# Kernel optimization log

Measured on AMD Instinct MI355X. Metric: run time of the kernel, lower is better.

The kernel has to match this reference:

```python
import jax, jax.numpy as jnp
import numpy as np

B, S, T = 1024, 1024, 32
TAGS = ["O"] + [p + f"T{i}" for i in range(1, 16) for p in ("B-", "I-")] + ["B-T16"]
MASKED = -1.0e4


def _init_params(key):
    bound = float(np.sqrt(6.0 / T))
    k1, k2, k3 = jax.random.split(key, 3)
    start = np.array(jax.random.uniform(k1, (T,), minval=-bound, maxval=bound))
    trans = np.array(jax.random.uniform(k2, (T, T), minval=-bound, maxval=bound))
    end = np.array(jax.random.uniform(k3, (T,), minval=-bound, maxval=bound))
    # structural BIO masking, as in _initialize_parameters
    for i, src in enumerate(TAGS):
        if src.startswith("I-"):
            start[i] = MASKED
        for j, tgt in enumerate(TAGS):
            if (src.startswith("B-") or src.startswith("I-")) and tgt.startswith("I-") and src[2:] != tgt[2:]:
                trans[i, j] = MASKED
            elif src == "O" and tgt.startswith("I-"):
                trans[i, j] = MASKED
    return jnp.asarray(start, jnp.float32), jnp.asarray(trans, jnp.float32), jnp.asarray(end, jnp.float32)


def setup_inputs() -> dict:
    key = jax.random.key(0)
    k_em, k_tag, k_len, k_par = jax.random.split(key, 4)
    emissions = jax.random.normal(k_em, (B, S, T), dtype=jnp.float32)
    tags = jax.random.randint(k_tag, (B, S), 0, T, dtype=jnp.int64) if jax.config.jax_enable_x64 else jax.random.randint(k_tag, (B, S), 0, T).astype(jnp.int32)
    lengths = jax.random.randint(k_len, (B,), S // 4, S + 1)
    mask = jnp.arange(S)[None, :] < lengths[:, None]  # prefix mask, bool [B, S]
    start_transitions, transitions, end_transitions = _init_params(k_par)
    return {
        "emissions": emissions,
        "tags": tags,
        "mask": mask,
        "start_transitions": start_transitions,
        "transitions": transitions,
        "end_transitions": end_transitions,
    }


def reference(emissions, tags, mask, start_transitions, transitions, end_transitions):
    b, s, t = emissions.shape
    ar = jnp.arange(s)
    bidx = jnp.arange(b)
    head = jnp.min(jnp.where(mask, ar[None, :], s - 1), axis=1)  # [B]
    tail = jnp.max(ar[None, :] * mask, axis=1)                   # [B]
    nonempty = mask.sum(axis=1) != 0

    # condition[:, j-1] == (mask[:, j] and head != j), for j = 1..S-1
    cond = mask[:, 1:] & (head[:, None] != ar[None, 1:])  # [B, S-1]

    # ---- numerator (gold path score): additive, fully vectorized ----
    head_tags = tags[bidx, head]
    tail_tags = tags[bidx, tail]
    em_tag = jnp.take_along_axis(emissions, tags[:, :, None], axis=2)[:, :, 0]  # [B, S]
    trans_step = transitions[tags[:, :-1], tags[:, 1:]]                          # [B, S-1]
    numerator = (start_transitions[head_tags]
                 + em_tag[bidx, head]
                 + jnp.sum(jnp.where(cond, trans_step + em_tag[:, 1:], 0.0), axis=1)
                 + end_transitions[tail_tags])
    numerator = jnp.where(nonempty, numerator, 0.0)

    # ---- denominator (log partition): scan over time ----
    score0 = start_transitions[None, :] + emissions[bidx, head]  # [B, T]

    def step(score, xs):
        em_j, cond_j = xs  # [B, T], [B]
        nxt = jax.nn.logsumexp(score[:, :, None] + transitions[None, :, :] + em_j[:, None, :], axis=1)
        return jnp.where(cond_j[:, None], nxt, score), None

    em_seq = jnp.moveaxis(emissions[:, 1:, :], 1, 0)  # [S-1, B, T]
    cond_seq = jnp.moveaxis(cond, 1, 0)               # [S-1, B]
    score_final, _ = jax.lax.scan(step, score0, (em_seq, cond_seq))
    denominator = jax.nn.logsumexp(score_final + end_transitions[None, :], axis=1)
    denominator = jnp.where(nonempty, denominator, 0.0)

    # ---- token_mean reduction ----
    llh = denominator - numerator
    labels = mask.sum(axis=1).astype(emissions.dtype)
    eps = 1e-6
    return jnp.sum(llh / (labels + eps)) / (jnp.sum(labels != 0).astype(emissions.dtype) + eps)
```

## Files before the change

### kernel.cpp

```cpp
#include <hip/hip_runtime.h>
#include <cstdint>

static constexpr int S = 1024;
static constexpr int T = 32;
static constexpr float L2E  = 1.4426950408889634f;
static constexpr float LN2f = 0.6931471805599453f;

typedef __attribute__((ext_vector_type(8)))  short  short8;
typedef __attribute__((ext_vector_type(16))) float  float16;

union Frag { unsigned u[4]; short8 s; };

__global__ void crf_zero(float* ws) {
  ws[0] = 0.0f; ws[1] = 0.0f; ((unsigned*)ws)[2] = 0u;
}

__device__ __forceinline__ float bcast_lane(float v, int k) {
  return __uint_as_float((unsigned)__builtin_amdgcn_readlane((int)__float_as_uint(v), k));
}

__device__ __forceinline__ unsigned cvtpk(float lo, float hi) {
  unsigned r;
  asm("v_cvt_pk_bf16_f32 %0, %1, %2" : "=v"(r) : "v"(lo), "v"(hi));
  return r;
}

__device__ __forceinline__ int sig(int k) {
  int g2 = (k >> 2) & 3;
  if (g2 == 1) g2 = 2; else if (g2 == 2) g2 = 1;
  return (k & ~12) | (g2 << 2);
}

__global__ __launch_bounds__(512, 8) void crf_main(
    const float* __restrict__ em, const int* __restrict__ tags,
    const int* __restrict__ mask, const float* __restrict__ startT,
    const float* __restrict__ trans, const float* __restrict__ endT,
    float* __restrict__ ws, float* __restrict__ out, int B)
{
  __shared__ __align__(16) float    s_g32[8 * 512];
  __shared__ __align__(16) unsigned s_mats[8 * 544];
  __shared__ float s_trans[1024];
  __shared__ short s_tags[1024];
  __shared__ unsigned long long s_mb[17];
  __shared__ int   s_head, s_tail, s_cnt, s_K[8];
  __shared__ float s_num[8];

  const int tid = threadIdx.x;
  const int l   = tid & 63;
  const int wv  = tid >> 6;
  const int b   = blockIdx.x;
  const int n   = l & 31;
  const int h   = l >> 5;

  const float* emb   = em   + (size_t)b * S * T;
  const int*   maskb = mask + (size_t)b * S;
  const int*   tagsb = tags + (size_t)b * S;

  for (int i = tid; i < 1024; i += 512) {
    s_tags[i]  = (short)tagsb[i];
    s_trans[i] = trans[i];
  }
  {
    unsigned long long b0 = __ballot(maskb[wv * 128 + l] != 0);
    unsigned long long b1 = __ballot(maskb[wv * 128 + 64 + l] != 0);
    if (l == 0) { s_mb[2 * wv] = b0; s_mb[2 * wv + 1] = b1; }
    if (tid == 0) s_mb[16] = 0ull;
  }

  Frag Alo, Ahi;
  #pragma unroll
  for (int p = 0; p < 4; ++p) {
    int k0 = 8 * h + 2 * p;
    Alo.u[p] = cvtpk(exp2f(trans[sig(k0 + 0)      * T + n] * L2E),
                     exp2f(trans[sig(k0 + 1)      * T + n] * L2E));
    Ahi.u[p] = cvtpk(exp2f(trans[sig(16 + k0 + 0) * T + n] * L2E),
                     exp2f(trans[sig(16 + k0 + 1) * T + n] * L2E));
  }
  __syncthreads();

  if (wv == 0) {
    int first = 0x7fffffff, last = -1, pc = 0;
    if (l < 16) {
      unsigned long long w = s_mb[l];
      if (w) {
        first = 64 * l + (int)__builtin_ctzll(w);
        last  = 64 * l + 63 - (int)__builtin_clzll(w);
        pc    = (int)__builtin_popcountll(w);
      }
    }
    #pragma unroll
    for (int d = 1; d < 64; d <<= 1) {
      first = min(first, __shfl_xor(first, d));
      last  = max(last,  __shfl_xor(last,  d));
      pc   += __shfl_xor(pc, d);
    }
    if (l == 0) { s_head = first; s_tail = last; s_cnt = pc; }
  }
  __syncthreads();
  const int cnt  = s_cnt;
  const int head = (cnt > 0) ? s_head : 0;
  const int tail = (cnt > 0) ? s_tail : 0;

  const int span = tail - head;
  const int Lc   = (span + 7) >> 3;
  const int c0   = head + 1 + wv * Lc;
  const int c1   = min(c0 + Lc, tail + 1);

  float* sgw32 = s_g32 + wv * 512;
  Frag Blo, Bhi;
  #pragma unroll
  for (int p = 0; p < 4; ++p) {
    int k0 = 8 * h + 2 * p;
    Blo.u[p] = ((sig(k0) == n)          ? 0x3F80u : 0u) |
               ((sig(k0 + 1) == n)      ? 0x3F800000u : 0u);
    Bhi.u[p] = ((sig(16 + k0) == n)     ? 0x3F80u : 0u) |
               ((sig(16 + k0 + 1) == n) ? 0x3F800000u : 0u);
  }
  int   Kacc  = 0;
  float numer = 0.0f;

  float4 v0, v1;
#define LOADEM(J0) do {                                                      \
    const int r0_ = min((J0) + (l >> 3),     S - 1);                         \
    const int r1_ = min((J0) + 8 + (l >> 3), S - 1);                         \
    v0 = ((const float4*)(emb + (size_t)r0_ * T))[l & 7];                    \
    v1 = ((const float4*)(emb + (size_t)r1_ * T))[l & 7];                    \
  } while (0)

#define STOREG() do {                                                        \
    float4 g0_, g1_;                                                         \
    g0_.x = exp2f(v0.x * L2E); g0_.y = exp2f(v0.y * L2E);                    \
    g0_.z = exp2f(v0.z * L2E); g0_.w = exp2f(v0.w * L2E);                    \
    g1_.x = exp2f(v1.x * L2E); g1_.y = exp2f(v1.y * L2E);                    \
    g1_.z = exp2f(v1.z * L2E); g1_.w = exp2f(v1.w * L2E);                    \
    ((float4*)sgw32)[l] = g0_; ((float4*)sgw32)[l + 64] = g1_;               \
  } while (0)

#define FOLD(JJ, RSC) do {                                                   \
    const float4* gw = (const float4*)(sgw32 + (JJ) * 32);                   \
    float4 wa = gw[h], wb = gw[h + 2], wc = gw[h + 4], wd = gw[h + 6];       \
    float16 D = {0,0,0,0,0,0,0,0,0,0,0,0,0,0,0,0};                           \
    D = __builtin_amdgcn_mfma_f32_32x32x16_bf16(Alo.s, Blo.s, D, 0, 0, 0);   \
    D = __builtin_amdgcn_mfma_f32_32x32x16_bf16(Ahi.s, Bhi.s, D, 0, 0, 0);   \
    D[0]  *= wa.x; D[1]  *= wa.y; D[2]  *= wa.z; D[3]  *= wa.w;              \
    D[4]  *= wb.x; D[5]  *= wb.y; D[6]  *= wb.z; D[7]  *= wb.w;              \
    D[8]  *= wc.x; D[9]  *= wc.y; D[10] *= wc.z; D[11] *= wc.w;              \
    D[12] *= wd.x; D[13] *= wd.y; D[14] *= wd.z; D[15] *= wd.w;              \
    if (RSC) {                                                               \
      float mx = fmaxf(fmaxf(fmaxf(D[0], D[1]), fmaxf(D[2], D[3])),          \
                       fmaxf(fmaxf(D[4], D[5]), fmaxf(D[6], D[7])));         \
      mx = fmaxf(mx, fmaxf(fmaxf(fmaxf(D[8], D[9]),  fmaxf(D[10], D[11])),   \
                           fmaxf(fmaxf(D[12], D[13]), fmaxf(D[14], D[15]))));\
      mx = fmaxf(mx, __shfl_xor(mx, 32));             \
      mx = __uint_as_float((unsigned)__builtin_amdgcn_readfirstlane(         \
               (int)__float_as_uint(mx)));                                   \
      int E = (int)((__float_as_uint(mx) >> 23) & 0xffu);                    \
      float sc = __uint_as_float((unsigned)(254 - E) << 23);                 \
      Kacc += E - 127;                                                       \
      _Pragma("unroll")                                                      \
      for (int q_ = 0; q_ < 16; ++q_) D[q_] *= sc;                           \
    }                                                                        \
    Blo.u[0] = cvtpk(D[0],  D[1]);  Blo.u[1] = cvtpk(D[2],  D[3]);           \
    Blo.u[2] = cvtpk(D[4],  D[5]);  Blo.u[3] = cvtpk(D[6],  D[7]);           \
    Bhi.u[0] = cvtpk(D[8],  D[9]);  Bhi.u[1] = cvtpk(D[10], D[11]);          \
    Bhi.u[2] = cvtpk(D[12], D[13]); Bhi.u[3] = cvtpk(D[14], D[15]);          \
  } while (0)

  if (c0 < c1) LOADEM(c0);

  for (int j0 = c0; j0 < c1; j0 += 16) {
    const int ns = min(16, c1 - j0);

    STOREG();
    if (j0 + 16 < c1) LOADEM(j0 + 16);

    const int w = j0 >> 6, o = j0 & 63;
    unsigned long long bits = s_mb[w] >> o;
    if (o) bits |= s_mb[w + 1] << (64 - o);
    unsigned eff = (unsigned)(bits & 0xFFFFull) & (unsigned)((1u << ns) - 1u);

    if (l < ns && ((eff >> l) & 1u)) {
      int j  = j0 + l;
      int tg = (int)s_tags[j], tp = (int)s_tags[j - 1];
      float gval = sgw32[l * 32 + tg];
      numer += s_trans[tp * T + tg] + log2f(gval) * LN2f;
    }

    if (eff == 0xFFFFu) {
      #pragma unroll
      for (int jj = 0; jj < 16; ++jj) FOLD(jj, ((jj & 7) == 7));
    } else {
      for (int jj = 0; jj < ns; ++jj)
        if ((eff >> jj) & 1u) FOLD(jj, true);
    }
  }
#undef FOLD
#undef STOREG
#undef LOADEM

  {
    unsigned* mw = s_mats + wv * 544;
    #pragma unroll
    for (int p = 0; p < 4; ++p) {
      mw[(sig(8 * h + 2 * p)      >> 1) * 34 + n] = Blo.u[p];
      mw[(sig(16 + 8 * h + 2 * p) >> 1) * 34 + n] = Bhi.u[p];
    }
  }
  #pragma unroll
  for (int d = 1; d < 64; d <<= 1) numer += __shfl_xor(numer, d);
  if (l == 0) { s_num[wv] = numer; s_K[wv] = Kacc; }
  __syncthreads();

  if (wv == 0) {
    const int t = n;
    const float em0 = emb[head * T + t];
    float sc0 = (startT[t] + em0) * L2E;
    float m0 = sc0;
    #pragma unroll
    for (int d = 1; d < 32; d <<= 1) m0 = fmaxf(m0, __shfl_xor(m0, d));
    float e = exp2f(sc0 - m0);
    float Mtot = m0;

    const unsigned sh = (t & 1) ? 0u : 16u;
    for (int c = 0; c < 8; ++c) {
      const unsigned* mw = s_mats + c * 544 + (t >> 1) * 34;
      float acc = 0.0f;
      #pragma unroll
      for (int q2 = 0; q2 < 16; ++q2) {
        uint2 w2 = *(const uint2*)(mw + 2 * q2);
        float vlo = __uint_as_float((w2.x << sh) & 0xFFFF0000u);
        float vhi = __uint_as_float((w2.y << sh) & 0xFFFF0000u);
        acc = fmaf(vlo, bcast_lane(e, 2 * q2), acc);
        acc = fmaf(vhi, bcast_lane(e, 2 * q2 + 1), acc);
      }
      e = acc;
      Mtot += (float)s_K[c];
      float mx = e;
      #pragma unroll
      for (int d = 1; d < 32; d <<= 1) mx = fmaxf(mx, __shfl_xor(mx, d));
      int E = (int)((__float_as_uint(mx) >> 23) & 0xffu);
      e *= __uint_as_float((unsigned)(254 - E) << 23);
      Mtot += (float)(E - 127);
    }

    float fv = e * exp2f(endT[t] * L2E);
    #pragma unroll
    for (int d = 1; d < 32; d <<= 1) fv += __shfl_xor(fv, d);
    float denom = (Mtot + log2f(fv)) * LN2f;

    if (l == 0) {
      if (cnt > 0) {
        float ntot = 0.0f;
        for (int wq = 0; wq < 8; ++wq) ntot += s_num[wq];
        int th = (int)s_tags[head], tt = (int)s_tags[tail];
        ntot += startT[th] + bcast_lane(em0, th) + endT[tt];
        atomicAdd(&ws[0], (denom - ntot) / ((float)cnt + 1e-6f));
        atomicAdd(&ws[1], 1.0f);
      }
      __threadfence();
      unsigned done = atomicAdd((unsigned*)ws + 2, 1u);
      if (done == (unsigned)(B - 1)) {
        __threadfence();
        out[0] = ws[0] / (ws[1] + 1e-6f);
      }
    }
  }
}

extern "C" void kernel_launch(void* const* d_in, const int* in_sizes, int n_in,
                              void* d_out, int out_size, void* d_ws, size_t ws_size,
                              hipStream_t stream) {
  const float* em     = (const float*)d_in[0];
  const int*   tags   = (const int*)d_in[1];
  const int*   mask   = (const int*)d_in[2];
  const float* startT = (const float*)d_in[3];
  const float* trans  = (const float*)d_in[4];
  const float* endT   = (const float*)d_in[5];
  float* out = (float*)d_out;
  float* ws  = (float*)d_ws;

  const int B = in_sizes[0] / (S * T);

  crf_zero<<<1, 1, 0, stream>>>(ws);
  crf_main<<<B, 512, 0, stream>>>(em, tags, mask, startT, trans, endT, ws, out, B);
}
```

Measured before the change: 268.4 us.

## Stream emission chunks directly into LDS with double-buffered global_load_lds

Replaces the register-staged emission prefetch (global load to VGPRs, exp, store to LDS) with direct global-to-LDS async loads into a per-wave double buffer of 8 timesteps, then exponentiates in place. The chunk size drops from 16 to 8 steps, and the MFMA now takes a constant zero accumulator. The aim is to free registers and overlap memory with the fold chain. In exchange it adds a full vmcnt wait each chunk, an extra LDS read/write pass, and lowers the launch-bounds occupancy hint from 8 to 6.

```diff
diff --git a/kernel.cpp b/kernel.cpp
--- a/kernel.cpp
+++ b/kernel.cpp
@@ -25,13 +25,20 @@
   return r;
 }
 
+__device__ __forceinline__ void gload16(const float* src, float* dst) {
+  __builtin_amdgcn_global_load_lds(
+      (const __attribute__((address_space(1))) unsigned int*)(src),
+      (__attribute__((address_space(3))) unsigned int*)(dst),
+      16, 0, 0);
+}
+
 __device__ __forceinline__ int sig(int k) {
   int g2 = (k >> 2) & 3;
   if (g2 == 1) g2 = 2; else if (g2 == 2) g2 = 1;
   return (k & ~12) | (g2 << 2);
 }
 
-__global__ __launch_bounds__(512, 8) void crf_main(
+__global__ __launch_bounds__(512, 6) void crf_main(
     const float* __restrict__ em, const int* __restrict__ tags,
     const int* __restrict__ mask, const float* __restrict__ startT,
     const float* __restrict__ trans, const float* __restrict__ endT,
@@ -106,7 +113,9 @@
   const int c0   = head + 1 + wv * Lc;
   const int c1   = min(c0 + Lc, tail + 1);
 
-  float* sgw32 = s_g32 + wv * 512;
+  float* bcur = s_g32 + wv * 512;
+  float* bnxt = bcur + 256;
+
   Frag Blo, Bhi;
   #pragma unroll
   for (int p = 0; p < 4; ++p) {
@@ -118,29 +127,12 @@
   }
   int   Kacc  = 0;
   float numer = 0.0f;
-
-  float4 v0, v1;
-#define LOADEM(J0) do {                                                      \
-    const int r0_ = min((J0) + (l >> 3),     S - 1);                         \
-    const int r1_ = min((J0) + 8 + (l >> 3), S - 1);                         \
-    v0 = ((const float4*)(emb + (size_t)r0_ * T))[l & 7];                    \
-    v1 = ((const float4*)(emb + (size_t)r1_ * T))[l & 7];                    \
-  } while (0)
-
-#define STOREG() do {                                                        \
-    float4 g0_, g1_;                                                         \
-    g0_.x = exp2f(v0.x * L2E); g0_.y = exp2f(v0.y * L2E);                    \
-    g0_.z = exp2f(v0.z * L2E); g0_.w = exp2f(v0.w * L2E);                    \
-    g1_.x = exp2f(v1.x * L2E); g1_.y = exp2f(v1.y * L2E);                    \
-    g1_.z = exp2f(v1.z * L2E); g1_.w = exp2f(v1.w * L2E);                    \
-    ((float4*)sgw32)[l] = g0_; ((float4*)sgw32)[l + 64] = g1_;               \
-  } while (0)
+  const float16 Zv = {0,0,0,0,0,0,0,0,0,0,0,0,0,0,0,0};
 
 #define FOLD(JJ, RSC) do {                                                   \
-    const float4* gw = (const float4*)(sgw32 + (JJ) * 32);                   \
+    const float4* gw = (const float4*)(gp + (JJ) * 32);                      \
     float4 wa = gw[h], wb = gw[h + 2], wc = gw[h + 4], wd = gw[h + 6];       \
-    float16 D = {0,0,0,0,0,0,0,0,0,0,0,0,0,0,0,0};                           \
-    D = __builtin_amdgcn_mfma_f32_32x32x16_bf16(Alo.s, Blo.s, D, 0, 0, 0);   \
+    float16 D = __builtin_amdgcn_mfma_f32_32x32x16_bf16(Alo.s, Blo.s, Zv, 0, 0, 0); \
     D = __builtin_amdgcn_mfma_f32_32x32x16_bf16(Ahi.s, Bhi.s, D, 0, 0, 0);   \
     D[0]  *= wa.x; D[1]  *= wa.y; D[2]  *= wa.z; D[3]  *= wa.w;              \
     D[4]  *= wb.x; D[5]  *= wb.y; D[6]  *= wb.z; D[7]  *= wb.w;              \
@@ -166,37 +158,54 @@
     Bhi.u[2] = cvtpk(D[12], D[13]); Bhi.u[3] = cvtpk(D[14], D[15]);          \
   } while (0)
 
-  if (c0 < c1) LOADEM(c0);
-
-  for (int j0 = c0; j0 < c1; j0 += 16) {
-    const int ns = min(16, c1 - j0);
-
-    STOREG();
-    if (j0 + 16 < c1) LOADEM(j0 + 16);
+  if (c0 < c1) {
+    const int base = min(c0, S - 8);
+    gload16(emb + (size_t)base * T + 4 * l, bcur);
+  }
+
+  for (int j0 = c0; j0 < c1; j0 += 8) {
+    const int ns   = min(8, c1 - j0);
+    const int base = min(j0, S - 8);
+    const int d    = j0 - base;
+
+    asm volatile("s_waitcnt vmcnt(0)" ::: "memory");
+    {
+      float4 r = ((const float4*)bcur)[l];
+      r.x = exp2f(r.x * L2E); r.y = exp2f(r.y * L2E);
+      r.z = exp2f(r.z * L2E); r.w = exp2f(r.w * L2E);
+      ((float4*)bcur)[l] = r;
+    }
+
+    if (j0 + 8 < c1) {
+      const int nb = min(j0 + 8, S - 8);
+      gload16(emb + (size_t)nb * T + 4 * l, bnxt);
+    }
+
+    const float* gp = bcur + d * 32;
 
     const int w = j0 >> 6, o = j0 & 63;
     unsigned long long bits = s_mb[w] >> o;
     if (o) bits |= s_mb[w + 1] << (64 - o);
-    unsigned eff = (unsigned)(bits & 0xFFFFull) & (unsigned)((1u << ns) - 1u);
+    unsigned eff = (unsigned)(bits & 0xFFull) & (unsigned)((1u << ns) - 1u);
 
     if (l < ns && ((eff >> l) & 1u)) {
       int j  = j0 + l;
       int tg = (int)s_tags[j], tp = (int)s_tags[j - 1];
-      float gval = sgw32[l * 32 + tg];
+      float gval = gp[l * 32 + tg];
       numer += s_trans[tp * T + tg] + log2f(gval) * LN2f;
     }
 
-    if (eff == 0xFFFFu) {
+    if (eff == 0xFFu) {
       #pragma unroll
-      for (int jj = 0; jj < 16; ++jj) FOLD(jj, ((jj & 7) == 7));
+      for (int jj = 0; jj < 8; ++jj) FOLD(jj, (jj == 7));
     } else {
       for (int jj = 0; jj < ns; ++jj)
         if ((eff >> jj) & 1u) FOLD(jj, true);
     }
+
+    float* tmp = bcur; bcur = bnxt; bnxt = tmp;
   }
 #undef FOLD
-#undef STOREG
-#undef LOADEM
 
   {
     unsigned* mw = s_mats + wv * 544;
```

Measured after the change: 270.6 us. No clear change (+0.8%).
